# Performance work log

Measured on AMD Instinct MI355X. Metric: run time of the kernel, lower is better.

The kernel has to match this reference:

```python
import jax, jax.numpy as jnp
import numpy as np
from jax import lax

IMG, P, C, D, H, L, B = 256, 16, 3, 768, 12, 8, 2
G = IMG // P            # 16
N = G * G               # 256 patches
FF = 2048               # hard-coded FFN hidden dim in ViTBlockWithCCAttention
DH = D // H
EPS = 1e-5


def setup_inputs() -> dict:
    key = jax.random.key(0)
    ks = jax.random.split(key, 24)
    s = 0.02
    rn = lambda k, shp: jax.random.normal(k, shp, jnp.float32) * s
    inp = {
        "x": jax.random.normal(ks[0], (B, C, IMG, IMG), jnp.float32),
        "patch_w": rn(ks[1], (D, C * P * P)),
        "patch_b": rn(ks[2], (D,)),
        "pos_embed": rn(ks[3], (1, N, D)),
        # per-layer stacked params (shared nn.MultiheadAttention per block)
        "in_proj_w": rn(ks[4], (L, 3 * D, D)),
        "in_proj_b": rn(ks[5], (L, 3 * D)),
        "out_w": rn(ks[6], (L, D, D)),
        "out_b": rn(ks[7], (L, D)),
        "ln1_g": jnp.ones((L, D), jnp.float32),
        "ln1_b": jnp.zeros((L, D), jnp.float32),
        "ln2_g": jnp.ones((L, D), jnp.float32),
        "ln2_b": jnp.zeros((L, D), jnp.float32),
        "ffn_w1": rn(ks[8], (L, FF, D)),
        "ffn_b1": rn(ks[9], (L, FF)),
        "ffn_w2": rn(ks[10], (L, D, FF)),
        "ffn_b2": rn(ks[11], (L, D)),
        "edge_w": rn(ks[12], (D, 1)),
        "edge_b": rn(ks[13], (D,)),
        "conv1_w": rn(ks[14], (256, D, 3, 3)),
        "conv1_b": rn(ks[15], (256,)),
        "conv2_w": rn(ks[16], (1, 256, 1, 1)),
        "conv2_b": rn(ks[17], (1,)),
    }
    return inp


def _ln(z, g, b):
    m = z.mean(-1, keepdims=True)
    v = ((z - m) ** 2).mean(-1, keepdims=True)
    return (z - m) / jnp.sqrt(v + EPS) * g + b


def _mha(z, wi, bi, wo, bo):
    # z: (M, S, D). Returns out (M,S,D) and head-averaged attn weights (M,S,S)
    M, S, _ = z.shape
    qkv = z @ wi.T + bi
    q, k, v = jnp.split(qkv, 3, axis=-1)
    sp = lambda t: t.reshape(M, S, H, DH).transpose(0, 2, 1, 3)  # (M,H,S,dh)
    q, k, v = sp(q), sp(k), sp(v)
    a = jax.nn.softmax(jnp.einsum('mhqd,mhkd->mhqk', q, k) / np.sqrt(DH).astype(np.float32), axis=-1)
    o = jnp.einsum('mhqk,mhkd->mhqd', a, v).transpose(0, 2, 1, 3).reshape(M, S, D)
    return o @ wo.T + bo, a.mean(1)


def reference(x, patch_w, patch_b, pos_embed, in_proj_w, in_proj_b, out_w, out_b,
              ln1_g, ln1_b, ln2_g, ln2_b, ffn_w1, ffn_b1, ffn_w2, ffn_b2,
              edge_w, edge_b, conv1_w, conv1_b, conv2_w, conv2_b):
    Bc = x.shape[0]
    # patch embedding: unfold -> (B, N, C*P*P) -> linear
    patches = x.reshape(Bc, C, G, P, G, P).transpose(0, 2, 4, 1, 3, 5).reshape(Bc, N, C * P * P)
    h = patches @ patch_w.T + patch_b + pos_embed

    edge_sum = jnp.zeros((Bc, N, D), h.dtype)
    for i in range(L):
        xl = _ln(h, ln1_g[i], ln1_b[i])
        x2d = xl.reshape(Bc, G, G, D)
        # rows: sequences along height, one per column
        row_x = x2d.transpose(0, 2, 1, 3).reshape(Bc * G, G, D)
        row_out, row_a = _mha(row_x, in_proj_w[i], in_proj_b[i], out_w[i], out_b[i])
        # cols: sequences along width, one per row
        col_x = x2d.reshape(Bc * G, G, D)
        col_out, col_a = _mha(col_x, in_proj_w[i], in_proj_b[i], out_w[i], out_b[i])
        attn_out = (row_out.reshape(Bc, G, G, D).transpose(0, 2, 1, 3)
                    + col_out.reshape(Bc, G, G, D)).reshape(Bc, N, D)
        h = h + attn_out
        z = _ln(h, ln2_g[i], ln2_b[i])
        h = h + jax.nn.relu(z @ ffn_w1[i].T + ffn_b1[i]) @ ffn_w2[i].T + ffn_b2[i]
        # attention-divergence edge tokens (query-averaged attn maps)
        div = jnp.abs(row_a.mean(1) - col_a.mean(1)).reshape(Bc, N, 1)
        edge_sum = edge_sum + (div @ edge_w.T + edge_b)
    h = h + edge_sum / L

    feat = h.transpose(0, 2, 1).reshape(Bc, D, G, G)
    feat = jax.image.resize(feat, (Bc, D, IMG, IMG), method="bilinear")  # align_corners=False
    dn = ("NCHW", "OIHW", "NCHW")
    y = lax.conv_general_dilated(feat, conv1_w, (1, 1), "SAME", dimension_numbers=dn)
    y = jax.nn.relu(y + conv1_b[None, :, None, None])
    y = lax.conv_general_dilated(y, conv2_w, (1, 1), "SAME", dimension_numbers=dn)
    return y + conv2_b[None, :, None, None]
```

## Files before the change

kernel.cpp:

```cpp
#include <hip/hip_runtime.h>
#include <hip/hip_bf16.h>
#include <math.h>

#define BB 2
#define CIN 3
#define IMGS 256
#define PS 16
#define GG 16
#define NN 256
#define DIM 768
#define NH 12
#define NL 8
#define FFD 2048
#define LNEPS 1e-5f

typedef __attribute__((ext_vector_type(8))) short bf16x8;
typedef __attribute__((ext_vector_type(4))) float f32x4;

#define MB     1
#define MB2    2
#define MPOS   4
#define MRELU  8
#define MRES   16
#define MOBF16 32
#define MAS2   64
#define MBF32  128
#define MLNA   256
#define MAIM2  512

__device__ inline unsigned short bc(float f) {
    return __builtin_bit_cast(unsigned short, __float2bfloat16(f));
}

__device__ inline void gload16(const unsigned short* g, unsigned short* l) {
    __builtin_amdgcn_global_load_lds((const __attribute__((address_space(1))) void*)g,
                                     (__attribute__((address_space(3))) void*)l, 16, 0, 0);
}

template<int MODE>
__global__ __launch_bounds__(256) void gemm_bf16(
    const void* __restrict__ Av, const void* __restrict__ A2v, const void* __restrict__ Bv,
    const float* __restrict__ bias, const float* __restrict__ pos,
    const float2* __restrict__ stats, const float* __restrict__ lng,
    const float* __restrict__ lnb,
    float* __restrict__ C, unsigned short* __restrict__ C16,
    int M, int N, int K, int zdiv,
    long long sAo, long long sBi, long long sCo, long long sCi)
{
    int z = blockIdx.y;
    int zo = z / zdiv, zi = z % zdiv;
    const unsigned short* A16 = (const unsigned short*)Av + (size_t)zo * sAo;
    const float* Af  = (const float*)Av  + (size_t)zo * sAo;
    const float* Af2 = (const float*)A2v + (size_t)zo * sAo;
    const unsigned short* B16 = (const unsigned short*)Bv + (size_t)zi * sBi;
    const float* Bf  = (const float*)Bv  + (size_t)zi * sBi;
    long long coff = (long long)zo * sCo + (long long)zi * sCi;

    int NBY = M >> 5;
    int nbysh = 31 - __builtin_clz(NBY);
    int id = blockIdx.x;
    int xcd = id & 7, q = id >> 3;
    int by = q & (NBY - 1), bxh = q >> nbysh;
    int bx = bxh * 8 + xcd;
    int bm = by * 32, bn = bx * 32;

    __shared__ __align__(16) unsigned short As[2][2048], Bs[2][2048];
    int tid = threadIdx.x;
    int lane = tid & 63, wave = tid >> 6;
    int wr = wave >> 1, wc = wave & 1;
    int s = wave * 64 + lane;
    int srow = s >> 3, schk = (s & 7) ^ (srow & 7);

    f32x4 acc = {};
    f32x4 rA0, rA1, rA20, rA21, rB0, rB1, gv0, gv1, bv0, bv1;
    float2 strow;

    auto gstageA = [&](int b, int kt) {
        gload16(A16 + (size_t)(bm + srow) * K + kt * 64 + schk * 8, &As[b][s * 8]);
    };
    auto gstageB = [&](int b, int kt) {
        gload16(B16 + (size_t)(bn + srow) * K + kt * 64 + schk * 8, &Bs[b][s * 8]);
    };
    auto ldA = [&](int kt) {
        int k0 = kt * 64 + schk * 8;
        if constexpr (MODE & MAIM2) {
            int m = bm + srow;
            int bq = m >> 8, n = m & 255, gy = n >> 4, gx = n & 15;
            int c = k0 >> 8, rem = k0 & 255, py = rem >> 4, px = rem & 15;
            const float* src = Af + (((size_t)(bq * CIN + c) * IMGS + gy * PS + py) << 8)
                             + gx * PS + px;
            rA0 = *(const f32x4*)(src);
            rA1 = *(const f32x4*)(src + 4);
        } else {
            size_t off = (size_t)(bm + srow) * K + k0;
            rA0 = *(const f32x4*)(Af + off);
            rA1 = *(const f32x4*)(Af + off + 4);
            if constexpr (MODE & MAS2) {
                rA20 = *(const f32x4*)(Af2 + off);
                rA21 = *(const f32x4*)(Af2 + off + 4);
            }
            if constexpr (MODE & MLNA) {
                strow = stats[bm + srow];
                gv0 = *(const f32x4*)(lng + k0); gv1 = *(const f32x4*)(lng + k0 + 4);
                bv0 = *(const f32x4*)(lnb + k0); bv1 = *(const f32x4*)(lnb + k0 + 4);
            }
        }
    };
    auto ldB = [&](int kt) {
        size_t off = (size_t)(bn + srow) * K + kt * 64 + schk * 8;
        rB0 = *(const f32x4*)(Bf + off);
        rB1 = *(const f32x4*)(Bf + off + 4);
    };
    auto wrA = [&](int b) {
        bf16x8 v;
        #pragma unroll
        for (int j = 0; j < 4; ++j) {
            float x0 = rA0[j], x1 = rA1[j];
            if constexpr (MODE & MAS2) { x0 += rA20[j]; x1 += rA21[j]; }
            if constexpr (MODE & MLNA) {
                x0 = (x0 - strow.x) * strow.y * gv0[j] + bv0[j];
                x1 = (x1 - strow.x) * strow.y * gv1[j] + bv1[j];
            }
            v[j] = (short)bc(x0); v[4 + j] = (short)bc(x1);
        }
        *(bf16x8*)(&As[b][s * 8]) = v;
    };
    auto wrB = [&](int b) {
        bf16x8 v;
        #pragma unroll
        for (int j = 0; j < 4; ++j) {
            v[j] = (short)bc(rB0[j]); v[4 + j] = (short)bc(rB1[j]);
        }
        *(bf16x8*)(&Bs[b][s * 8]) = v;
    };
    constexpr bool regA = (MODE & (MAS2 | MLNA | MAIM2)) != 0;
    auto compute = [&](int b) {
        const unsigned short* Ab = As[b];
        const unsigned short* Bb = Bs[b];
        int rl = lane & 15, kh = lane >> 4;
        #pragma unroll
        for (int ks = 0; ks < 2; ++ks) {
            int kc = ks * 4 + kh;
            int ar = 16 * wr + rl, br = 16 * wc + rl;
            bf16x8 af = *(const bf16x8*)(Ab + ar * 64 + (kc ^ (ar & 7)) * 8);
            bf16x8 bf = *(const bf16x8*)(Bb + br * 64 + (kc ^ (br & 7)) * 8);
            acc = __builtin_amdgcn_mfma_f32_16x16x32_bf16(af, bf, acc, 0, 0, 0);
        }
    };

    int nt = K >> 6;
    if constexpr (!regA) gstageA(0, 0); else { ldA(0); wrA(0); }
    if constexpr (!(MODE & MBF32)) gstageB(0, 0); else { ldB(0); wrB(0); }
    __syncthreads();
    int buf = 0;
    for (int t = 0; t < nt; ++t) {
        if (t + 1 < nt) {
            if constexpr (!regA) gstageA(buf ^ 1, t + 1); else ldA(t + 1);
            if constexpr (!(MODE & MBF32)) gstageB(buf ^ 1, t + 1); else ldB(t + 1);
        }
        compute(buf);
        if (t + 1 < nt) {
            if constexpr (regA) wrA(buf ^ 1);
            if constexpr (MODE & MBF32) wrB(buf ^ 1);
        }
        __syncthreads();
        buf ^= 1;
    }

    #pragma unroll
    for (int r = 0; r < 4; ++r) {
        int row = bm + 16 * wr + (lane >> 4) * 4 + r;
        int col = bn + 16 * wc + (lane & 15);
        float v = acc[r];
        if (MODE & (MB | MB2)) v += bias[col] * ((MODE & MB2) ? 2.f : 1.f);
        if (MODE & MPOS) v += pos[(size_t)(row & (NN - 1)) * N + col];
        if (MODE & MRELU) v = fmaxf(v, 0.f);
        long long ci = coff + (long long)row * N + col;
        if (MODE & MOBF16) C16[ci] = bc(v);
        else if (MODE & MRES) C[ci] += v;
        else C[ci] = v;
    }
}

__global__ void wct_kernel(const float* __restrict__ w, unsigned short* __restrict__ Wct)
{
    int idx = blockIdx.x * 256 + threadIdx.x;
    int c = idx % DIM;
    int t = idx / DIM;
    int oc = t & 255;
    int dydx = t >> 8;
    int dy = dydx / 3, dx = dydx % 3;
    Wct[idx] = bc(w[((size_t)(oc * DIM + c) * 3 + dy) * 3 + dx]);
}

__global__ __launch_bounds__(256) void lnstat_kernel(const float* __restrict__ X,
                                                     float2* __restrict__ st)
{
    int row = blockIdx.x * 4 + (threadIdx.x >> 6);
    int lane = threadIdx.x & 63;
    const float* xp = X + (size_t)row * DIM + lane * 4;
    float s = 0.f, s2 = 0.f;
    #pragma unroll
    for (int seg = 0; seg < 3; ++seg) {
        f32x4 v = *(const f32x4*)(xp + seg * 256);
        s += v[0] + v[1] + v[2] + v[3];
        s2 += v[0] * v[0] + v[1] * v[1] + v[2] * v[2] + v[3] * v[3];
    }
    #pragma unroll
    for (int off = 32; off > 0; off >>= 1) {
        s  += __shfl_xor(s, off);
        s2 += __shfl_xor(s2, off);
    }
    if (lane == 0) {
        float mean = s * (1.f / DIM);
        float var = s2 * (1.f / DIM) - mean * mean;
        st[row] = make_float2(mean, rsqrtf(var + LNEPS));
    }
}

__global__ __launch_bounds__(256) void attn_kernel(
    const float* __restrict__ qkv, float* __restrict__ orow,
    float* __restrict__ ocol, float* __restrict__ amh)
{
    int b = blockIdx.x >> 4, g = blockIdx.x & 15;
    int type = blockIdx.y;
    int hh = blockIdx.z;
    int tid = threadIdx.x;
    __shared__ float qs[16][68], ks[16][68], vs[16][68], as_[16][17];
    {
        int sr = tid >> 4, dq = tid & 15;
        int n = (type == 0) ? (sr * GG + g) : (g * GG + sr);
        const float* base = qkv + (size_t)(b * NN + n) * (3 * DIM) + hh * 64 + dq * 4;
        float4 qv = *(const float4*)(base);
        float4 kv = *(const float4*)(base + DIM);
        float4 vv = *(const float4*)(base + 2 * DIM);
        *(float4*)&qs[sr][dq * 4] = qv;
        *(float4*)&ks[sr][dq * 4] = kv;
        *(float4*)&vs[sr][dq * 4] = vv;
    }
    __syncthreads();
    int s = tid >> 4, t = tid & 15;
    float sc = 0.f;
    #pragma unroll
    for (int d = 0; d < 64; ++d) sc += qs[s][d] * ks[t][d];
    sc *= 0.125f;
    float mx = sc;
    #pragma unroll
    for (int off = 1; off < 16; off <<= 1) mx = fmaxf(mx, __shfl_xor(mx, off, 16));
    float p = __expf(sc - mx);
    float sum = p;
    #pragma unroll
    for (int off = 1; off < 16; off <<= 1) sum += __shfl_xor(sum, off, 16);
    as_[s][t] = p / sum;
    __syncthreads();
    if (tid < 16) {
        float a = 0.f;
        #pragma unroll
        for (int ss = 0; ss < 16; ++ss) a += as_[ss][tid];
        amh[((size_t)(type * BB + b) * NN + g * GG + tid) * NH + hh] = a;
    }
    int s2 = tid >> 4, dg = (tid & 15) * 4;
    float o0 = 0, o1 = 0, o2 = 0, o3 = 0;
    #pragma unroll
    for (int t2 = 0; t2 < 16; ++t2) {
        float a2 = as_[s2][t2];
        o0 += a2 * vs[t2][dg];
        o1 += a2 * vs[t2][dg + 1];
        o2 += a2 * vs[t2][dg + 2];
        o3 += a2 * vs[t2][dg + 3];
    }
    int n2 = (type == 0) ? (s2 * GG + g) : (g * GG + s2);
    float* op = ((type == 0) ? orow : ocol) + (size_t)(b * NN + n2) * DIM + hh * 64 + dg;
    *(float4*)op = make_float4(o0, o1, o2, o3);
}

__global__ void divred_kernel(const float* __restrict__ amh, float* __restrict__ divacc)
{
    int i = blockIdx.x * 256 + threadIdx.x;
    int b = i >> 8, n = i & 255;
    float acc = 0.f;
    #pragma unroll
    for (int l = 0; l < NL; ++l) {
        float rs = 0.f, cs = 0.f;
        const float* base = amh + (size_t)l * 12288 + (size_t)b * 3072 + n * 12;
        #pragma unroll
        for (int h = 0; h < NH; ++h) {
            rs += base[h];
            cs += base[6144 + h];
        }
        acc += fabsf(rs - cs);
    }
    divacc[i] = acc * (1.f / (NH * GG));
}

__global__ void hfin_kernel(const float* __restrict__ h, const float* __restrict__ divacc,
                            const float* __restrict__ ew, const float* __restrict__ eb,
                            unsigned short* __restrict__ hf)
{
    int idx = blockIdx.x * 256 + threadIdx.x;
    int d = idx % DIM, m = idx / DIM;
    hf[idx] = bc(h[idx] + divacc[m] * (1.f / NL) * ew[d] + eb[d]);
}

__global__ __launch_bounds__(256) void s_kernel(const float* __restrict__ P, float* __restrict__ S)
{
    int bdy = blockIdx.y;
    int b = bdy / 3, dy = bdy % 3;
    int ocg = blockIdx.x;
    __shared__ float Pl[3][4][16][17];
    int tid = threadIdx.x;
    #pragma unroll
    for (int l = 0; l < 12; ++l) {
        int e = l * 256 + tid;
        int dx = e >> 10, rem = e & 1023;
        int oc = rem >> 8, pix = rem & 255;
        int i = pix >> 4, j = pix & 15;
        Pl[dx][oc][j][i] =
            P[(((size_t)b * 9 + dy * 3 + dx) * 256 + ocg * 4 + oc) * 256 + pix];
    }
    __syncthreads();
    int xq = tid >> 6, oc = (tid >> 4) & 3, i = tid & 15;
    for (int xx = 0; xx < 64; ++xx) {
        int x = xq * 64 + xx;
        float acc = 0.f;
        #pragma unroll
        for (int dx = 0; dx < 3; ++dx) {
            int u = x + dx - 1;
            float p = (u + 0.5f) * 0.0625f - 0.5f;
            float fl = floorf(p);
            float f = p - fl;
            int j0 = (int)fl;
            int ja = j0 < 0 ? 0 : j0;
            int jb = (j0 + 1 > 15) ? 15 : (j0 + 1);
            bool valid = (u >= 0) && (u <= 255);
            float w0 = valid ? 1.f - f : 0.f;
            float w1 = valid ? f : 0.f;
            acc += w0 * Pl[dx][oc][ja][i] + w1 * Pl[dx][oc][jb][i];
        }
        S[(((size_t)(b * 256 + x) * 3 + dy) * 256 + ocg * 4 + oc) * 16 + i] = acc;
    }
}

__global__ __launch_bounds__(256) void out_kernel(
    const float* __restrict__ S, const float* __restrict__ b1,
    const float* __restrict__ w2, const float* __restrict__ b2p,
    float* __restrict__ out)
{
    int b = blockIdx.x >> 8, x = blockIdx.x & 255;
    __shared__ float Sl[12288];
    const float* Sp = S + (size_t)(b * 256 + x) * 12288;
    for (int l = threadIdx.x; l < 12288; l += 256) Sl[l] = Sp[l];
    __syncthreads();
    int y = threadIdx.x;
    float wy[3][2];
    int iy[3][2];
    #pragma unroll
    for (int dy = 0; dy < 3; ++dy) {
        int v = y + dy - 1;
        if (v < 0 || v > 255) {
            wy[dy][0] = wy[dy][1] = 0.f;
            iy[dy][0] = iy[dy][1] = 0;
        } else {
            float pp = (v + 0.5f) * 0.0625f - 0.5f;
            float fl = floorf(pp);
            float f = pp - fl;
            int i0 = (int)fl;
            iy[dy][0] = i0 < 0 ? 0 : i0;
            iy[dy][1] = (i0 + 1 > 15) ? 15 : (i0 + 1);
            wy[dy][0] = 1.f - f;
            wy[dy][1] = f;
        }
    }
    float acc = 0.f;
    for (int oc = 0; oc < 256; ++oc) {
        float sv = 0.f;
        #pragma unroll
        for (int dy = 0; dy < 3; ++dy)
            sv += wy[dy][0] * Sl[dy * 4096 + oc * 16 + iy[dy][0]]
                + wy[dy][1] * Sl[dy * 4096 + oc * 16 + iy[dy][1]];
        sv += b1[oc];
        acc += fmaxf(sv, 0.f) * w2[oc];
    }
    out[(size_t)b * 65536 + y * 256 + x] = acc + b2p[0];
}

extern "C" void kernel_launch(void* const* d_in, const int* in_sizes, int n_in,
                              void* d_out, int out_size, void* d_ws, size_t ws_size,
                              hipStream_t stream)
{
    const float* x         = (const float*)d_in[0];
    const float* patch_w   = (const float*)d_in[1];
    const float* patch_b   = (const float*)d_in[2];
    const float* pos_embed = (const float*)d_in[3];
    const float* in_proj_w = (const float*)d_in[4];
    const float* in_proj_b = (const float*)d_in[5];
    const float* out_w     = (const float*)d_in[6];
    const float* out_b     = (const float*)d_in[7];
    const float* ln1_g     = (const float*)d_in[8];
    const float* ln1_b     = (const float*)d_in[9];
    const float* ln2_g     = (const float*)d_in[10];
    const float* ln2_b     = (const float*)d_in[11];
    const float* ffn_w1    = (const float*)d_in[12];
    const float* ffn_b1    = (const float*)d_in[13];
    const float* ffn_w2    = (const float*)d_in[14];
    const float* ffn_b2    = (const float*)d_in[15];
    const float* edge_w    = (const float*)d_in[16];
    const float* edge_b    = (const float*)d_in[17];
    const float* conv1_w   = (const float*)d_in[18];
    const float* conv1_b   = (const float*)d_in[19];
    const float* conv2_w   = (const float*)d_in[20];
    const float* conv2_b   = (const float*)d_in[21];
    float* out = (float*)d_out;
    float* ws = (float*)d_ws;

    float* h      = ws;
    float* qkv    = h + 393216;
    float* orow   = qkv + 1179648;
    float* ocol   = orow + 393216;
    float* Pb     = ocol + 393216;
    float* Sb     = Pb + 1179648;
    float* amh    = Sb + 6291456;
    float* divacc = amh + 98304;
    float2* stats = (float2*)(divacc + 512);
    unsigned short* hid16  = (unsigned short*)(divacc + 512 + 1024);
    unsigned short* hfin16 = hid16 + 1048576;
    unsigned short* Wct16  = hfin16 + 393216;

    wct_kernel<<<dim3(6912), 256, 0, stream>>>(conv1_w, Wct16);
    gemm_bf16<MB | MPOS | MAIM2 | MBF32><<<dim3(24 * 16), 256, 0, stream>>>(
        x, nullptr, patch_w, patch_b, pos_embed, nullptr, nullptr, nullptr,
        h, nullptr, 512, 768, 768, 1, 0, 0, 0, 0);

    for (int l = 0; l < NL; ++l) {
        lnstat_kernel<<<dim3(128), 256, 0, stream>>>(h, stats);
        gemm_bf16<MB | MLNA | MBF32><<<dim3(72 * 16), 256, 0, stream>>>(
            h, nullptr, in_proj_w + (size_t)l * 1769472,
            in_proj_b + (size_t)l * 2304, nullptr, stats,
            ln1_g + l * DIM, ln1_b + l * DIM, qkv, nullptr,
            512, 2304, 768, 1, 0, 0, 0, 0);
        attn_kernel<<<dim3(BB * GG, 2, NH), 256, 0, stream>>>(
            qkv, orow, ocol, amh + (size_t)l * 12288);
        gemm_bf16<MB2 | MRES | MAS2 | MBF32><<<dim3(24 * 16), 256, 0, stream>>>(
            orow, ocol, out_w + (size_t)l * 589824,
            out_b + (size_t)l * DIM, nullptr, nullptr, nullptr, nullptr,
            h, nullptr, 512, 768, 768, 1, 0, 0, 0, 0);
        lnstat_kernel<<<dim3(128), 256, 0, stream>>>(h, stats);
        gemm_bf16<MB | MRELU | MOBF16 | MLNA | MBF32><<<dim3(64 * 16), 256, 0, stream>>>(
            h, nullptr, ffn_w1 + (size_t)l * 1572864,
            ffn_b1 + (size_t)l * FFD, nullptr, stats,
            ln2_g + l * DIM, ln2_b + l * DIM, nullptr, hid16,
            512, 2048, 768, 1, 0, 0, 0, 0);
        gemm_bf16<MB | MRES | MBF32><<<dim3(24 * 16), 256, 0, stream>>>(
            hid16, nullptr, ffn_w2 + (size_t)l * 1572864,
            ffn_b2 + (size_t)l * DIM, nullptr, nullptr, nullptr, nullptr,
            h, nullptr, 512, 768, 2048, 1, 0, 0, 0, 0);
    }

    divred_kernel<<<dim3(2), 256, 0, stream>>>(amh, divacc);
    hfin_kernel<<<dim3(1536), 256, 0, stream>>>(h, divacc, edge_w, edge_b, hfin16);
    gemm_bf16<0><<<dim3(8 * 8, 18), 256, 0, stream>>>(
        Wct16, nullptr, hfin16, nullptr, nullptr, nullptr, nullptr, nullptr,
        Pb, nullptr, 256, 256, 768,
        2, 196608LL, 196608LL, 65536LL, 589824LL);
    s_kernel<<<dim3(64, 6), 256, 0, stream>>>(Pb, Sb);
    out_kernel<<<dim3(512), 256, 0, stream>>>(Sb, conv1_b, conv2_w, conv2_b, out);
}
```

Measured before the change: 677.5 us.

## Fuse LayerNorm statistics into GEMM epilogues and merge divergence reduction kernels

Residual-producing GEMMs now accumulate per-row sum and sum-of-squares into a stats buffer through wave shuffles and atomics. The consuming LN-fused GEMM derives mean and rstd from these sums, which removes the two standalone lnstat kernels per layer. The divergence reduction is folded into hfin_kernel, which now processes one row per block. This cuts 17 kernel launches and their extra passes over h, at the cost of atomics, a memset, and one-pass variance that is slightly less numerically stable.

```diff
diff --git a/kernel.cpp b/kernel.cpp
--- a/kernel.cpp
+++ b/kernel.cpp
@@ -27,6 +27,7 @@
 #define MBF32  128
 #define MLNA   256
 #define MAIM2  512
+#define MSTAT  1024
 
 __device__ inline unsigned short bc(float f) {
     return __builtin_bit_cast(unsigned short, __float2bfloat16(f));
@@ -42,7 +43,7 @@
     const void* __restrict__ Av, const void* __restrict__ A2v, const void* __restrict__ Bv,
     const float* __restrict__ bias, const float* __restrict__ pos,
     const float2* __restrict__ stats, const float* __restrict__ lng,
-    const float* __restrict__ lnb,
+    const float* __restrict__ lnb, float2* __restrict__ statsOut,
     float* __restrict__ C, unsigned short* __restrict__ C16,
     int M, int N, int K, int zdiv,
     long long sAo, long long sBi, long long sCo, long long sCi)
@@ -100,7 +101,10 @@
                 rA21 = *(const f32x4*)(Af2 + off + 4);
             }
             if constexpr (MODE & MLNA) {
-                strow = stats[bm + srow];
+                float2 sraw = stats[bm + srow];
+                float mean = sraw.x * (1.f / DIM);
+                float var = sraw.y * (1.f / DIM) - mean * mean;
+                strow = make_float2(mean, rsqrtf(var + LNEPS));
                 gv0 = *(const f32x4*)(lng + k0); gv1 = *(const f32x4*)(lng + k0 + 4);
                 bv0 = *(const f32x4*)(lnb + k0); bv1 = *(const f32x4*)(lnb + k0 + 4);
             }
@@ -167,6 +171,7 @@
         buf ^= 1;
     }
 
+    float vfin[4];
     #pragma unroll
     for (int r = 0; r < 4; ++r) {
         int row = bm + 16 * wr + (lane >> 4) * 4 + r;
@@ -176,9 +181,26 @@
         if (MODE & MPOS) v += pos[(size_t)(row & (NN - 1)) * N + col];
         if (MODE & MRELU) v = fmaxf(v, 0.f);
         long long ci = coff + (long long)row * N + col;
-        if (MODE & MOBF16) C16[ci] = bc(v);
-        else if (MODE & MRES) C[ci] += v;
-        else C[ci] = v;
+        if (MODE & MOBF16) { C16[ci] = bc(v); }
+        else if (MODE & MRES) { v += C[ci]; C[ci] = v; }
+        else { C[ci] = v; }
+        vfin[r] = v;
+    }
+    if constexpr (MODE & MSTAT) {
+        #pragma unroll
+        for (int r = 0; r < 4; ++r) {
+            float sv = vfin[r], s2 = vfin[r] * vfin[r];
+            #pragma unroll
+            for (int m = 1; m < 16; m <<= 1) {
+                sv += __shfl_xor(sv, m);
+                s2 += __shfl_xor(s2, m);
+            }
+            if ((lane & 15) == 0) {
+                int row = bm + 16 * wr + (lane >> 4) * 4 + r;
+                atomicAdd(&((float*)&statsOut[row])[0], sv);
+                atomicAdd(&((float*)&statsOut[row])[1], s2);
+            }
+        }
     }
 }
 
@@ -191,31 +213,6 @@
     int dydx = t >> 8;
     int dy = dydx / 3, dx = dydx % 3;
     Wct[idx] = bc(w[((size_t)(oc * DIM + c) * 3 + dy) * 3 + dx]);
-}
-
-__global__ __launch_bounds__(256) void lnstat_kernel(const float* __restrict__ X,
-                                                     float2* __restrict__ st)
-{
-    int row = blockIdx.x * 4 + (threadIdx.x >> 6);
-    int lane = threadIdx.x & 63;
-    const float* xp = X + (size_t)row * DIM + lane * 4;
-    float s = 0.f, s2 = 0.f;
-    #pragma unroll
-    for (int seg = 0; seg < 3; ++seg) {
-        f32x4 v = *(const f32x4*)(xp + seg * 256);
-        s += v[0] + v[1] + v[2] + v[3];
-        s2 += v[0] * v[0] + v[1] * v[1] + v[2] * v[2] + v[3] * v[3];
-    }
-    #pragma unroll
-    for (int off = 32; off > 0; off >>= 1) {
-        s  += __shfl_xor(s, off);
-        s2 += __shfl_xor(s2, off);
-    }
-    if (lane == 0) {
-        float mean = s * (1.f / DIM);
-        float var = s2 * (1.f / DIM) - mean * mean;
-        st[row] = make_float2(mean, rsqrtf(var + LNEPS));
-    }
 }
 
 __global__ __launch_bounds__(256) void attn_kernel(
@@ -274,32 +271,38 @@
     *(float4*)op = make_float4(o0, o1, o2, o3);
 }
 
-__global__ void divred_kernel(const float* __restrict__ amh, float* __restrict__ divacc)
-{
-    int i = blockIdx.x * 256 + threadIdx.x;
-    int b = i >> 8, n = i & 255;
-    float acc = 0.f;
-    #pragma unroll
-    for (int l = 0; l < NL; ++l) {
+__global__ __launch_bounds__(256) void hfin_kernel(
+    const float* __restrict__ h, const float* __restrict__ amh,
+    const float* __restrict__ ew, const float* __restrict__ eb,
+    unsigned short* __restrict__ hf)
+{
+    int m = blockIdx.x;
+    int b = m >> 8, n = m & 255;
+    int tid = threadIdx.x;
+    __shared__ float divs;
+    if (tid < 8) {
+        const float* base = amh + (size_t)tid * 12288 + (size_t)b * 3072 + n * 12;
         float rs = 0.f, cs = 0.f;
-        const float* base = amh + (size_t)l * 12288 + (size_t)b * 3072 + n * 12;
-        #pragma unroll
-        for (int h = 0; h < NH; ++h) {
-            rs += base[h];
-            cs += base[6144 + h];
-        }
-        acc += fabsf(rs - cs);
-    }
-    divacc[i] = acc * (1.f / (NH * GG));
-}
-
-__global__ void hfin_kernel(const float* __restrict__ h, const float* __restrict__ divacc,
-                            const float* __restrict__ ew, const float* __restrict__ eb,
-                            unsigned short* __restrict__ hf)
-{
-    int idx = blockIdx.x * 256 + threadIdx.x;
-    int d = idx % DIM, m = idx / DIM;
-    hf[idx] = bc(h[idx] + divacc[m] * (1.f / NL) * ew[d] + eb[d]);
+        #pragma unroll
+        for (int hh = 0; hh < NH; ++hh) {
+            rs += base[hh];
+            cs += base[6144 + hh];
+        }
+        float d = fabsf(rs - cs);
+        d += __shfl_xor(d, 1);
+        d += __shfl_xor(d, 2);
+        d += __shfl_xor(d, 4);
+        if (tid == 0) divs = d * (1.f / (NH * GG)) * (1.f / NL);
+    }
+    __syncthreads();
+    float dv = divs;
+    const float* hp = h + (size_t)m * DIM;
+    unsigned short* yp = hf + (size_t)m * DIM;
+    #pragma unroll
+    for (int seg = 0; seg < 3; ++seg) {
+        int d0 = tid + seg * 256;
+        yp[d0] = bc(hp[d0] + dv * ew[d0] + eb[d0]);
+    }
 }
 
 __global__ __launch_bounds__(256) void s_kernel(const float* __restrict__ P, float* __restrict__ S)
@@ -420,47 +423,46 @@
     float* Pb     = ocol + 393216;
     float* Sb     = Pb + 1179648;
     float* amh    = Sb + 6291456;
-    float* divacc = amh + 98304;
-    float2* stats = (float2*)(divacc + 512);
-    unsigned short* hid16  = (unsigned short*)(divacc + 512 + 1024);
+    float2* statsA = (float2*)(amh + 98304);
+    unsigned short* hid16  = (unsigned short*)(amh + 98304 + 17408);
     unsigned short* hfin16 = hid16 + 1048576;
     unsigned short* Wct16  = hfin16 + 393216;
 
+    hipMemsetAsync(statsA, 0, 17 * 512 * sizeof(float2), stream);
     wct_kernel<<<dim3(6912), 256, 0, stream>>>(conv1_w, Wct16);
-    gemm_bf16<MB | MPOS | MAIM2 | MBF32><<<dim3(24 * 16), 256, 0, stream>>>(
+    gemm_bf16<MB | MPOS | MAIM2 | MBF32 | MSTAT><<<dim3(24 * 16), 256, 0, stream>>>(
         x, nullptr, patch_w, patch_b, pos_embed, nullptr, nullptr, nullptr,
-        h, nullptr, 512, 768, 768, 1, 0, 0, 0, 0);
+        statsA, h, nullptr, 512, 768, 768, 1, 0, 0, 0, 0);
 
     for (int l = 0; l < NL; ++l) {
-        lnstat_kernel<<<dim3(128), 256, 0, stream>>>(h, stats);
         gemm_bf16<MB | MLNA | MBF32><<<dim3(72 * 16), 256, 0, stream>>>(
             h, nullptr, in_proj_w + (size_t)l * 1769472,
-            in_proj_b + (size_t)l * 2304, nullptr, stats,
-            ln1_g + l * DIM, ln1_b + l * DIM, qkv, nullptr,
+            in_proj_b + (size_t)l * 2304, nullptr, statsA + (size_t)(2 * l) * 512,
+            ln1_g + l * DIM, ln1_b + l * DIM, nullptr, qkv, nullptr,
             512, 2304, 768, 1, 0, 0, 0, 0);
         attn_kernel<<<dim3(BB * GG, 2, NH), 256, 0, stream>>>(
             qkv, orow, ocol, amh + (size_t)l * 12288);
-        gemm_bf16<MB2 | MRES | MAS2 | MBF32><<<dim3(24 * 16), 256, 0, stream>>>(
+        gemm_bf16<MB2 | MRES | MAS2 | MBF32 | MSTAT><<<dim3(24 * 16), 256, 0, stream>>>(
             orow, ocol, out_w + (size_t)l * 589824,
             out_b + (size_t)l * DIM, nullptr, nullptr, nullptr, nullptr,
-            h, nullptr, 512, 768, 768, 1, 0, 0, 0, 0);
-        lnstat_kernel<<<dim3(128), 256, 0, stream>>>(h, stats);
+            statsA + (size_t)(2 * l + 1) * 512, h, nullptr,
+            512, 768, 768, 1, 0, 0, 0, 0);
         gemm_bf16<MB | MRELU | MOBF16 | MLNA | MBF32><<<dim3(64 * 16), 256, 0, stream>>>(
             h, nullptr, ffn_w1 + (size_t)l * 1572864,
-            ffn_b1 + (size_t)l * FFD, nullptr, stats,
-            ln2_g + l * DIM, ln2_b + l * DIM, nullptr, hid16,
+            ffn_b1 + (size_t)l * FFD, nullptr, statsA + (size_t)(2 * l + 1) * 512,
+            ln2_g + l * DIM, ln2_b + l * DIM, nullptr, nullptr, hid16,
             512, 2048, 768, 1, 0, 0, 0, 0);
-        gemm_bf16<MB | MRES | MBF32><<<dim3(24 * 16), 256, 0, stream>>>(
+        gemm_bf16<MB | MRES | MBF32 | MSTAT><<<dim3(24 * 16), 256, 0, stream>>>(
             hid16, nullptr, ffn_w2 + (size_t)l * 1572864,
             ffn_b2 + (size_t)l * DIM, nullptr, nullptr, nullptr, nullptr,
-            h, nullptr, 512, 768, 2048, 1, 0, 0, 0, 0);
-    }
-
-    divred_kernel<<<dim3(2), 256, 0, stream>>>(amh, divacc);
-    hfin_kernel<<<dim3(1536), 256, 0, stream>>>(h, divacc, edge_w, edge_b, hfin16);
+            statsA + (size_t)(2 * l + 2) * 512, h, nullptr,
+            512, 768, 2048, 1, 0, 0, 0, 0);
+    }
+
+    hfin_kernel<<<dim3(512), 256, 0, stream>>>(h, amh, edge_w, edge_b, hfin16);
     gemm_bf16<0><<<dim3(8 * 8, 18), 256, 0, stream>>>(
         Wct16, nullptr, hfin16, nullptr, nullptr, nullptr, nullptr, nullptr,
-        Pb, nullptr, 256, 256, 768,
+        nullptr, Pb, nullptr, 256, 256, 768,
         2, 196608LL, 196608LL, 65536LL, 589824LL);
     s_kernel<<<dim3(64, 6), 256, 0, stream>>>(Pb, Sb);
     out_kernel<<<dim3(512), 256, 0, stream>>>(Sb, conv1_b, conv2_w, conv2_b, out);
```

Measured after the change: 800.4 us. 18.1% more time.

## Template GEMM on N-tile width, widen QKV/FFN1 tiles, fuse divergence reduce into hfin

Applied to the files above, without the earlier changes.

Adds a BN template parameter so each block computes 32xBN with several MFMA accumulators that reuse the A fragment. The QKV and FFN1 projections switch to 64-wide tiles, which halves their block count and the repeated A loads with LayerNorm. Block-to-tile remapping changes from interleaved XCD striping to contiguous chunks per XCD. The separate divergence-reduction kernel is folded into hfin_kernel, removing one launch. The wider tiles leave fewer blocks and use more registers, which may reduce occupancy.

```diff
diff --git a/kernel.cpp b/kernel.cpp
--- a/kernel.cpp
+++ b/kernel.cpp
@@ -37,7 +37,7 @@
                                      (__attribute__((address_space(3))) void*)l, 16, 0, 0);
 }
 
-template<int MODE>
+template<int MODE, int BN>
 __global__ __launch_bounds__(256) void gemm_bf16(
     const void* __restrict__ Av, const void* __restrict__ A2v, const void* __restrict__ Bv,
     const float* __restrict__ bias, const float* __restrict__ pos,
@@ -47,6 +47,7 @@
     int M, int N, int K, int zdiv,
     long long sAo, long long sBi, long long sCo, long long sCi)
 {
+    constexpr int NI = BN / 32;
     int z = blockIdx.y;
     int zo = z / zdiv, zi = z % zdiv;
     const unsigned short* A16 = (const unsigned short*)Av + (size_t)zo * sAo;
@@ -59,32 +60,37 @@
     int NBY = M >> 5;
     int nbysh = 31 - __builtin_clz(NBY);
     int id = blockIdx.x;
-    int xcd = id & 7, q = id >> 3;
-    int by = q & (NBY - 1), bxh = q >> nbysh;
-    int bx = bxh * 8 + xcd;
-    int bm = by * 32, bn = bx * 32;
-
-    __shared__ __align__(16) unsigned short As[2][2048], Bs[2][2048];
+    int qch = gridDim.x >> 3;
+    int wgid = (id & 7) * qch + (id >> 3);
+    int bx = wgid >> nbysh, by = wgid & (NBY - 1);
+    int bm = by * 32, bn = bx * BN;
+
+    __shared__ __align__(16) unsigned short As[2][2048], Bs[2][BN * 64];
     int tid = threadIdx.x;
     int lane = tid & 63, wave = tid >> 6;
     int wr = wave >> 1, wc = wave & 1;
-    int s = wave * 64 + lane;
-    int srow = s >> 3, schk = (s & 7) ^ (srow & 7);
-
-    f32x4 acc = {};
-    f32x4 rA0, rA1, rA20, rA21, rB0, rB1, gv0, gv1, bv0, bv1;
+    int sA = tid;
+    int srowA = sA >> 3, schkA = (sA & 7) ^ (srowA & 7);
+
+    f32x4 acc[NI] = {};
+    f32x4 rA0, rA1, rA20, rA21, rB[NI][2], gv0, gv1, bv0, bv1;
     float2 strow;
 
     auto gstageA = [&](int b, int kt) {
-        gload16(A16 + (size_t)(bm + srow) * K + kt * 64 + schk * 8, &As[b][s * 8]);
+        gload16(A16 + (size_t)(bm + srowA) * K + kt * 64 + schkA * 8, &As[b][sA * 8]);
     };
     auto gstageB = [&](int b, int kt) {
-        gload16(B16 + (size_t)(bn + srow) * K + kt * 64 + schk * 8, &Bs[b][s * 8]);
+        #pragma unroll
+        for (int i = 0; i < NI; ++i) {
+            int s = tid + i * 256;
+            int row = s >> 3, chk = (s & 7) ^ (row & 7);
+            gload16(B16 + (size_t)(bn + row) * K + kt * 64 + chk * 8, &Bs[b][s * 8]);
+        }
     };
     auto ldA = [&](int kt) {
-        int k0 = kt * 64 + schk * 8;
+        int k0 = kt * 64 + schkA * 8;
         if constexpr (MODE & MAIM2) {
-            int m = bm + srow;
+            int m = bm + srowA;
             int bq = m >> 8, n = m & 255, gy = n >> 4, gx = n & 15;
             int c = k0 >> 8, rem = k0 & 255, py = rem >> 4, px = rem & 15;
             const float* src = Af + (((size_t)(bq * CIN + c) * IMGS + gy * PS + py) << 8)
@@ -92,7 +98,7 @@
             rA0 = *(const f32x4*)(src);
             rA1 = *(const f32x4*)(src + 4);
         } else {
-            size_t off = (size_t)(bm + srow) * K + k0;
+            size_t off = (size_t)(bm + srowA) * K + k0;
             rA0 = *(const f32x4*)(Af + off);
             rA1 = *(const f32x4*)(Af + off + 4);
             if constexpr (MODE & MAS2) {
@@ -100,16 +106,21 @@
                 rA21 = *(const f32x4*)(Af2 + off + 4);
             }
             if constexpr (MODE & MLNA) {
-                strow = stats[bm + srow];
+                strow = stats[bm + srowA];
                 gv0 = *(const f32x4*)(lng + k0); gv1 = *(const f32x4*)(lng + k0 + 4);
                 bv0 = *(const f32x4*)(lnb + k0); bv1 = *(const f32x4*)(lnb + k0 + 4);
             }
         }
     };
     auto ldB = [&](int kt) {
-        size_t off = (size_t)(bn + srow) * K + kt * 64 + schk * 8;
-        rB0 = *(const f32x4*)(Bf + off);
-        rB1 = *(const f32x4*)(Bf + off + 4);
+        #pragma unroll
+        for (int i = 0; i < NI; ++i) {
+            int s = tid + i * 256;
+            int row = s >> 3, chk = (s & 7) ^ (row & 7);
+            size_t off = (size_t)(bn + row) * K + kt * 64 + chk * 8;
+            rB[i][0] = *(const f32x4*)(Bf + off);
+            rB[i][1] = *(const f32x4*)(Bf + off + 4);
+        }
     };
     auto wrA = [&](int b) {
         bf16x8 v;
@@ -123,15 +134,19 @@
             }
             v[j] = (short)bc(x0); v[4 + j] = (short)bc(x1);
         }
-        *(bf16x8*)(&As[b][s * 8]) = v;
+        *(bf16x8*)(&As[b][sA * 8]) = v;
     };
     auto wrB = [&](int b) {
-        bf16x8 v;
-        #pragma unroll
-        for (int j = 0; j < 4; ++j) {
-            v[j] = (short)bc(rB0[j]); v[4 + j] = (short)bc(rB1[j]);
-        }
-        *(bf16x8*)(&Bs[b][s * 8]) = v;
+        #pragma unroll
+        for (int i = 0; i < NI; ++i) {
+            int s = tid + i * 256;
+            bf16x8 v;
+            #pragma unroll
+            for (int j = 0; j < 4; ++j) {
+                v[j] = (short)bc(rB[i][0][j]); v[4 + j] = (short)bc(rB[i][1][j]);
+            }
+            *(bf16x8*)(&Bs[b][s * 8]) = v;
+        }
     };
     constexpr bool regA = (MODE & (MAS2 | MLNA | MAIM2)) != 0;
     auto compute = [&](int b) {
@@ -141,10 +156,14 @@
         #pragma unroll
         for (int ks = 0; ks < 2; ++ks) {
             int kc = ks * 4 + kh;
-            int ar = 16 * wr + rl, br = 16 * wc + rl;
+            int ar = 16 * wr + rl;
             bf16x8 af = *(const bf16x8*)(Ab + ar * 64 + (kc ^ (ar & 7)) * 8);
-            bf16x8 bf = *(const bf16x8*)(Bb + br * 64 + (kc ^ (br & 7)) * 8);
-            acc = __builtin_amdgcn_mfma_f32_16x16x32_bf16(af, bf, acc, 0, 0, 0);
+            #pragma unroll
+            for (int ni = 0; ni < NI; ++ni) {
+                int br = 16 * NI * wc + 16 * ni + rl;
+                bf16x8 bf = *(const bf16x8*)(Bb + br * 64 + (kc ^ (br & 7)) * 8);
+                acc[ni] = __builtin_amdgcn_mfma_f32_16x16x32_bf16(af, bf, acc[ni], 0, 0, 0);
+            }
         }
     };
 
@@ -168,17 +187,20 @@
     }
 
     #pragma unroll
-    for (int r = 0; r < 4; ++r) {
-        int row = bm + 16 * wr + (lane >> 4) * 4 + r;
-        int col = bn + 16 * wc + (lane & 15);
-        float v = acc[r];
-        if (MODE & (MB | MB2)) v += bias[col] * ((MODE & MB2) ? 2.f : 1.f);
-        if (MODE & MPOS) v += pos[(size_t)(row & (NN - 1)) * N + col];
-        if (MODE & MRELU) v = fmaxf(v, 0.f);
-        long long ci = coff + (long long)row * N + col;
-        if (MODE & MOBF16) C16[ci] = bc(v);
-        else if (MODE & MRES) C[ci] += v;
-        else C[ci] = v;
+    for (int ni = 0; ni < NI; ++ni) {
+        #pragma unroll
+        for (int r = 0; r < 4; ++r) {
+            int row = bm + 16 * wr + (lane >> 4) * 4 + r;
+            int col = bn + 16 * NI * wc + 16 * ni + (lane & 15);
+            float v = acc[ni][r];
+            if (MODE & (MB | MB2)) v += bias[col] * ((MODE & MB2) ? 2.f : 1.f);
+            if (MODE & MPOS) v += pos[(size_t)(row & (NN - 1)) * N + col];
+            if (MODE & MRELU) v = fmaxf(v, 0.f);
+            long long ci = coff + (long long)row * N + col;
+            if (MODE & MOBF16) C16[ci] = bc(v);
+            else if (MODE & MRES) C[ci] += v;
+            else C[ci] = v;
+        }
     }
 }
 
@@ -274,32 +296,38 @@
     *(float4*)op = make_float4(o0, o1, o2, o3);
 }
 
-__global__ void divred_kernel(const float* __restrict__ amh, float* __restrict__ divacc)
-{
-    int i = blockIdx.x * 256 + threadIdx.x;
-    int b = i >> 8, n = i & 255;
-    float acc = 0.f;
-    #pragma unroll
-    for (int l = 0; l < NL; ++l) {
+__global__ __launch_bounds__(256) void hfin_kernel(
+    const float* __restrict__ h, const float* __restrict__ amh,
+    const float* __restrict__ ew, const float* __restrict__ eb,
+    unsigned short* __restrict__ hf)
+{
+    int m = blockIdx.x;
+    int b = m >> 8, n = m & 255;
+    int tid = threadIdx.x;
+    __shared__ float divs;
+    if (tid < 8) {
+        const float* base = amh + (size_t)tid * 12288 + (size_t)b * 3072 + n * 12;
         float rs = 0.f, cs = 0.f;
-        const float* base = amh + (size_t)l * 12288 + (size_t)b * 3072 + n * 12;
-        #pragma unroll
-        for (int h = 0; h < NH; ++h) {
-            rs += base[h];
-            cs += base[6144 + h];
-        }
-        acc += fabsf(rs - cs);
-    }
-    divacc[i] = acc * (1.f / (NH * GG));
-}
-
-__global__ void hfin_kernel(const float* __restrict__ h, const float* __restrict__ divacc,
-                            const float* __restrict__ ew, const float* __restrict__ eb,
-                            unsigned short* __restrict__ hf)
-{
-    int idx = blockIdx.x * 256 + threadIdx.x;
-    int d = idx % DIM, m = idx / DIM;
-    hf[idx] = bc(h[idx] + divacc[m] * (1.f / NL) * ew[d] + eb[d]);
+        #pragma unroll
+        for (int hh = 0; hh < NH; ++hh) {
+            rs += base[hh];
+            cs += base[6144 + hh];
+        }
+        float d = fabsf(rs - cs);
+        d += __shfl_xor(d, 1);
+        d += __shfl_xor(d, 2);
+        d += __shfl_xor(d, 4);
+        if (tid == 0) divs = d * (1.f / (NH * GG)) * (1.f / NL);
+    }
+    __syncthreads();
+    float dv = divs;
+    const float* hp = h + (size_t)m * DIM;
+    unsigned short* yp = hf + (size_t)m * DIM;
+    #pragma unroll
+    for (int seg = 0; seg < 3; ++seg) {
+        int d0 = tid + seg * 256;
+        yp[d0] = bc(hp[d0] + dv * ew[d0] + eb[d0]);
+    }
 }
 
 __global__ __launch_bounds__(256) void s_kernel(const float* __restrict__ P, float* __restrict__ S)
@@ -420,45 +448,43 @@
     float* Pb     = ocol + 393216;
     float* Sb     = Pb + 1179648;
     float* amh    = Sb + 6291456;
-    float* divacc = amh + 98304;
-    float2* stats = (float2*)(divacc + 512);
-    unsigned short* hid16  = (unsigned short*)(divacc + 512 + 1024);
+    float2* stats = (float2*)(amh + 98304);
+    unsigned short* hid16  = (unsigned short*)(amh + 98304 + 1024);
     unsigned short* hfin16 = hid16 + 1048576;
     unsigned short* Wct16  = hfin16 + 393216;
 
     wct_kernel<<<dim3(6912), 256, 0, stream>>>(conv1_w, Wct16);
-    gemm_bf16<MB | MPOS | MAIM2 | MBF32><<<dim3(24 * 16), 256, 0, stream>>>(
+    gemm_bf16<MB | MPOS | MAIM2 | MBF32, 32><<<dim3(24 * 16), 256, 0, stream>>>(
         x, nullptr, patch_w, patch_b, pos_embed, nullptr, nullptr, nullptr,
         h, nullptr, 512, 768, 768, 1, 0, 0, 0, 0);
 
     for (int l = 0; l < NL; ++l) {
         lnstat_kernel<<<dim3(128), 256, 0, stream>>>(h, stats);
-        gemm_bf16<MB | MLNA | MBF32><<<dim3(72 * 16), 256, 0, stream>>>(
+        gemm_bf16<MB | MLNA | MBF32, 64><<<dim3(36 * 16), 256, 0, stream>>>(
             h, nullptr, in_proj_w + (size_t)l * 1769472,
             in_proj_b + (size_t)l * 2304, nullptr, stats,
             ln1_g + l * DIM, ln1_b + l * DIM, qkv, nullptr,
             512, 2304, 768, 1, 0, 0, 0, 0);
         attn_kernel<<<dim3(BB * GG, 2, NH), 256, 0, stream>>>(
             qkv, orow, ocol, amh + (size_t)l * 12288);
-        gemm_bf16<MB2 | MRES | MAS2 | MBF32><<<dim3(24 * 16), 256, 0, stream>>>(
+        gemm_bf16<MB2 | MRES | MAS2 | MBF32, 32><<<dim3(24 * 16), 256, 0, stream>>>(
             orow, ocol, out_w + (size_t)l * 589824,
             out_b + (size_t)l * DIM, nullptr, nullptr, nullptr, nullptr,
             h, nullptr, 512, 768, 768, 1, 0, 0, 0, 0);
         lnstat_kernel<<<dim3(128), 256, 0, stream>>>(h, stats);
-        gemm_bf16<MB | MRELU | MOBF16 | MLNA | MBF32><<<dim3(64 * 16), 256, 0, stream>>>(
+        gemm_bf16<MB | MRELU | MOBF16 | MLNA | MBF32, 64><<<dim3(32 * 16), 256, 0, stream>>>(
             h, nullptr, ffn_w1 + (size_t)l * 1572864,
             ffn_b1 + (size_t)l * FFD, nullptr, stats,
             ln2_g + l * DIM, ln2_b + l * DIM, nullptr, hid16,
             512, 2048, 768, 1, 0, 0, 0, 0);
-        gemm_bf16<MB | MRES | MBF32><<<dim3(24 * 16), 256, 0, stream>>>(
+        gemm_bf16<MB | MRES | MBF32, 32><<<dim3(24 * 16), 256, 0, stream>>>(
             hid16, nullptr, ffn_w2 + (size_t)l * 1572864,
             ffn_b2 + (size_t)l * DIM, nullptr, nullptr, nullptr, nullptr,
             h, nullptr, 512, 768, 2048, 1, 0, 0, 0, 0);
     }
 
-    divred_kernel<<<dim3(2), 256, 0, stream>>>(amh, divacc);
-    hfin_kernel<<<dim3(1536), 256, 0, stream>>>(h, divacc, edge_w, edge_b, hfin16);
-    gemm_bf16<0><<<dim3(8 * 8, 18), 256, 0, stream>>>(
+    hfin_kernel<<<dim3(512), 256, 0, stream>>>(h, amh, edge_w, edge_b, hfin16);
+    gemm_bf16<0, 32><<<dim3(8 * 8, 18), 256, 0, stream>>>(
         Wct16, nullptr, hfin16, nullptr, nullptr, nullptr, nullptr, nullptr,
         Pb, nullptr, 256, 256, 768,
         2, 196608LL, 196608LL, 65536LL, 589824LL);
```

Result: faster. 663.7 us (-2.0%).
